# Optimization experiments

Hardware: AMD Instinct MI355X
Metric: run time of the kernel (lower is better)

## Reference

```python
import jax, jax.numpy as jnp
import numpy as np

B, S, D, H = 2, 2048, 1024, 16
DEPTH = D // H


def setup_inputs() -> dict:
    key = jax.random.key(0)
    ks = jax.random.split(key, 8)
    w_scale = 0.02
    # causal mask: 1.0 where attention is NOT allowed (added as mask * -1e9)
    causal = jnp.triu(jnp.ones((S, S), dtype=jnp.float32), k=1)[None, None]  # [1,1,S,S]
    return {
        "q": jax.random.normal(ks[0], (B, S, D), dtype=jnp.float32),
        "k": jax.random.normal(ks[1], (B, S, D), dtype=jnp.float32),
        "v": jax.random.normal(ks[2], (B, S, D), dtype=jnp.float32),
        "mask": causal,
        "Wq": jax.random.normal(ks[3], (D, D), dtype=jnp.float32) * w_scale,
        "bq": jnp.zeros((D,), dtype=jnp.float32),
        "Wk": jax.random.normal(ks[4], (D, D), dtype=jnp.float32) * w_scale,
        "bk": jnp.zeros((D,), dtype=jnp.float32),
        "Wv": jax.random.normal(ks[5], (D, D), dtype=jnp.float32) * w_scale,
        "bv": jnp.zeros((D,), dtype=jnp.float32),
        "Wo": jax.random.normal(ks[6], (D, D), dtype=jnp.float32) * w_scale,
        "bo": jnp.zeros((D,), dtype=jnp.float32),
    }


def _split_heads(x):
    # [B,S,D] -> [B,H,S,depth]
    return x.reshape(B, S, H, DEPTH).transpose(0, 2, 1, 3)


def reference(q, k, v, mask, Wq, bq, Wk, bk, Wv, bv, Wo, bo):
    qh = _split_heads(q @ Wq + bq)
    kh = _split_heads(k @ Wk + bk)
    vh = _split_heads(v @ Wv + bv)
    scale = 1.0 / jnp.sqrt(jnp.asarray(DEPTH, dtype=qh.dtype))
    logits = jnp.einsum('bhqd,bhkd->bhqk', qh, kh) * scale  # [B,H,S,S]
    logits = logits + mask * (-1e9)
    attn = jax.nn.softmax(logits, axis=-1)
    out = jnp.einsum('bhqk,bhkd->bhqd', attn, vh)  # [B,H,S,depth]
    out = out.transpose(0, 2, 1, 3).reshape(B, S, D)
    return out @ Wo + bo
```

## Files before the change

kernel.cpp:

```cpp
#include <hip/hip_runtime.h>


typedef unsigned short u16;
typedef unsigned int u32;

using bf16x8 = __attribute__((ext_vector_type(8))) short;
using f32x4  = __attribute__((ext_vector_type(4))) float;

#define SEQ 2048
#define DMODEL 1024
#define NHEAD 16
#define DEPTH 64
#define BATCH 2
#define M_ROWS (BATCH * SEQ)

__device__ __forceinline__ u16 f2bf(float f) {
    union { float f; u32 u; } v; v.f = f;
    u32 u = v.u;
    return (u16)((u + 0x7FFFu + ((u >> 16) & 1u)) >> 16);
}
__device__ __forceinline__ u16 f2bf_trunc(float f) {
    union { float f; u32 u; } v; v.f = f;
    return (u16)(v.u >> 16);
}

__device__ __forceinline__ f32x4 mfma16(bf16x8 a, bf16x8 b, f32x4 c) {
    return __builtin_amdgcn_mfma_f32_16x16x32_bf16(a, b, c, 0, 0, 0);
}

__device__ __forceinline__ void glds16(const u16* src, u16* dst) {
    __builtin_amdgcn_global_load_lds((const __attribute__((address_space(1))) void*)src,
                                     (__attribute__((address_space(3))) void*)dst,
                                     16, 0, 0);
}

__device__ __forceinline__ bf16x8 fragld(const u16* base, int lr, int gc) {
    return *(const bf16x8*)(base + lr * 64 + (((gc ^ lr) & 7) << 3));
}

__global__ void cvt3_kernel(const float* __restrict__ q, const float* __restrict__ k,
                            const float* __restrict__ v,
                            u16* __restrict__ qo, u16* __restrict__ ko, u16* __restrict__ vo) {
    const float* in; u16* out;
    if (blockIdx.z == 0)      { in = q; out = qo; }
    else if (blockIdx.z == 1) { in = k; out = ko; }
    else                      { in = v; out = vo; }
    int idx = blockIdx.x * blockDim.x + threadIdx.x;
    float4 val = ((const float4*)in)[idx];
    ushort4 o;
    o.x = f2bf(val.x); o.y = f2bf(val.y); o.z = f2bf(val.z); o.w = f2bf(val.w);
    ((ushort4*)out)[idx] = o;
}

__global__ void wtrans_kernel(const float* __restrict__ Wq, const float* __restrict__ Wk,
                              const float* __restrict__ Wv, const float* __restrict__ Wo,
                              u16* __restrict__ Wqt, u16* __restrict__ Wkt,
                              u16* __restrict__ Wvt, u16* __restrict__ Wot) {
    __shared__ float tile[32][33];
    const float* W; u16* Wt;
    switch (blockIdx.z) {
        case 0: W = Wq; Wt = Wqt; break;
        case 1: W = Wk; Wt = Wkt; break;
        case 2: W = Wv; Wt = Wvt; break;
        default: W = Wo; Wt = Wot; break;
    }
    int k0 = blockIdx.x * 32, n0 = blockIdx.y * 32;
    int tx = threadIdx.x, ty = threadIdx.y;
#pragma unroll
    for (int i = 0; i < 4; ++i)
        tile[ty + 8 * i][tx] = W[(size_t)(k0 + ty + 8 * i) * DMODEL + n0 + tx];
    __syncthreads();
#pragma unroll
    for (int i = 0; i < 4; ++i)
        Wt[(size_t)(n0 + ty + 8 * i) * DMODEL + k0 + tx] = f2bf(tile[tx][ty + 8 * i]);
}

template<int TM>
__device__ __forceinline__ void gemm_core(const u16* __restrict__ A, const u16* __restrict__ Bt,
                                          const float* __restrict__ bias,
                                          u16* __restrict__ outb, float* __restrict__ outf,
                                          int mode, float oscale, int bm0, int bn0) {
    constexpr int K = DMODEL;
    constexpr int MI = TM / 32;
    __shared__ u16 As[TM * 64];
    __shared__ u16 Bs[128 * 64];
    int t = threadIdx.x;
    int w = t >> 6, lane = t & 63, l15 = lane & 15, quad = lane >> 4;
    int wm = (w >> 1) * (TM / 2), wn = (w & 1) * 64;
    int r8 = lane >> 3, g8 = lane & 7;
    int gswz = ((g8 ^ r8) << 3);
    f32x4 acc[MI][4] = {};

    for (int it = 0; it < K / 64; ++it) {
        int k0 = it * 64;
        __syncthreads();
#pragma unroll
        for (int c = 0; c < MI; ++c) {
            int ch = w * MI + c;
            glds16(A + (size_t)(bm0 + ch * 8 + r8) * K + k0 + gswz, As + ch * 512);
        }
#pragma unroll
        for (int c = 0; c < 4; ++c) {
            int ch = w * 4 + c;
            glds16(Bt + (size_t)(bn0 + ch * 8 + r8) * K + k0 + gswz, Bs + ch * 512);
        }
        __syncthreads();
#pragma unroll
        for (int kk = 0; kk < 2; ++kk) {
            bf16x8 af[MI], bfr[4];
#pragma unroll
            for (int i = 0; i < MI; ++i) af[i]  = fragld(As, wm + i * 16 + l15, kk * 4 + quad);
#pragma unroll
            for (int j = 0; j < 4;  ++j) bfr[j] = fragld(Bs, wn + j * 16 + l15, kk * 4 + quad);
#pragma unroll
            for (int i = 0; i < MI; ++i)
#pragma unroll
                for (int j = 0; j < 4; ++j)
                    acc[i][j] = mfma16(af[i], bfr[j], acc[i][j]);
        }
    }
#pragma unroll
    for (int i = 0; i < MI; ++i) {
        int row_g0 = bm0 + wm + i * 16 + quad * 4;
#pragma unroll
        for (int j = 0; j < 4; ++j) {
            int col_g = bn0 + wn + j * 16 + l15;
            float bsv = bias[col_g];
#pragma unroll
            for (int r = 0; r < 4; ++r) {
                float v = (acc[i][j][r] + bsv) * oscale;
                int rg = row_g0 + r;
                if (mode == 2) {
                    outf[(size_t)rg * DMODEL + col_g] = v;
                } else {
                    int b = rg >> 11, s = rg & (SEQ - 1);
                    int h = col_g >> 6, d = col_g & 63;
                    size_t idx;
                    if (mode == 0) idx = ((size_t)(b * NHEAD + h) * SEQ + s) * DEPTH + d;
                    else           idx = ((size_t)(b * NHEAD + h) * DEPTH + d) * SEQ + s;
                    outb[idx] = f2bf(v);
                }
            }
        }
    }
}

#define SCALE_Q 0.1803368801111204f

__global__ __launch_bounds__(256) void gemm_qkv(
        const u16* __restrict__ qb, const u16* __restrict__ kb, const u16* __restrict__ vb,
        const u16* __restrict__ Wqt, const u16* __restrict__ Wkt, const u16* __restrict__ Wvt,
        const float* __restrict__ bq, const float* __restrict__ bk, const float* __restrict__ bv,
        u16* __restrict__ Qp, u16* __restrict__ Kp, u16* __restrict__ Vpt) {
    int id = blockIdx.x;
    int c = id & 7, m = id >> 3;
    int slab = c * 12 + (m >> 3);
    int x = m & 7;
    int z = slab >> 5, y = slab & 31;
    int bm0 = y * 128, bn0 = x * 128;
    if (z == 0)      gemm_core<128>(qb, Wqt, bq, Qp,  nullptr, 0, SCALE_Q, bm0, bn0);
    else if (z == 1) gemm_core<128>(kb, Wkt, bk, Kp,  nullptr, 0, 1.0f,    bm0, bn0);
    else             gemm_core<128>(vb, Wvt, bv, Vpt, nullptr, 1, 1.0f,    bm0, bn0);
}

__global__ __launch_bounds__(256) void gemm_out(
        const u16* __restrict__ attnb, const u16* __restrict__ Wot,
        const float* __restrict__ bo, float* __restrict__ out) {
    int id = blockIdx.x;
    int c = id & 7, m = id >> 3;
    int slab = c * 8 + (m >> 3);
    int x = m & 7;
    gemm_core<64>(attnb, Wot, bo, nullptr, out, 2, 1.0f, slab * 64, x * 128);
}

#define LP 72
__global__ __launch_bounds__(256) void attn_kernel(
        const u16* __restrict__ Qp, const u16* __restrict__ Kp,
        const u16* __restrict__ Vpt, u16* __restrict__ attn_out, u32* __restrict__ ctrs) {
    __shared__ u16 Klds[2][64 * 64];
    __shared__ u16 Vtlds[2][64 * 64];
    __shared__ u16 Plds[4 * 16 * LP];
    __shared__ u32 item_s;
    int t = threadIdx.x, w = t >> 6, lane = t & 63, l15 = lane & 15, quad = lane >> 4;
    int r8 = lane >> 3, g8 = lane & 7;
    int gswz = ((g8 ^ r8) << 3);
    u16* Pw = Plds + w * 16 * LP;
    int xcd = blockIdx.x & 7;
    u32* my_ctr = ctrs + xcd * 32;

    bf16x8 ones;
#pragma unroll
    for (int i = 0; i < 8; ++i) ones[i] = (short)0x3F80;

    for (;;) {
        if (t == 0) item_s = atomicAdd(my_ctr, 1);
        __syncthreads();
        u32 item = item_s;
        if (item >= 128) break;
        int qt = 31 - (int)(item >> 2);
        int bh = xcd * 4 + (int)(item & 3);
        int q0 = qt * 64;
        int nkt = qt + 1;
        int b = bh >> 4, h = bh & 15;
        const u16* Qbase = Qp  + (size_t)bh * SEQ * DEPTH;
        const u16* Kbase = Kp  + (size_t)bh * SEQ * DEPTH;
        const u16* Vbase = Vpt + (size_t)bh * DEPTH * SEQ;

        int qrow = q0 + w * 16 + l15;
        bf16x8 qf[2];
        qf[0] = *(const bf16x8*)(Qbase + (size_t)qrow * DEPTH + quad * 8);
        qf[1] = *(const bf16x8*)(Qbase + (size_t)qrow * DEPTH + 32 + quad * 8);

        f32x4 of[4] = {};
        f32x4 lacc = {};

#pragma unroll
        for (int c2 = 0; c2 < 2; ++c2) {
            int ch = w * 2 + c2;
            glds16(Kbase + (size_t)(ch * 8 + r8) * DEPTH + gswz, Klds[0] + ch * 512);
            glds16(Vbase + (size_t)(ch * 8 + r8) * SEQ + gswz,   Vtlds[0] + ch * 512);
        }

        for (int kt = 0; kt < nkt; ++kt) {
            int cur = kt & 1;
            __syncthreads();
            if (kt + 1 < nkt) {
                int nx = cur ^ 1, kn = kt + 1;
#pragma unroll
                for (int c2 = 0; c2 < 2; ++c2) {
                    int ch = w * 2 + c2;
                    glds16(Kbase + (size_t)(kn * 64 + ch * 8 + r8) * DEPTH + gswz,
                           Klds[nx] + ch * 512);
                    glds16(Vbase + (size_t)(ch * 8 + r8) * SEQ + kn * 64 + gswz,
                           Vtlds[nx] + ch * 512);
                }
            }
            f32x4 sc[4] = {};
#pragma unroll
            for (int nt = 0; nt < 4; ++nt)
#pragma unroll
                for (int kk = 0; kk < 2; ++kk)
                    sc[nt] = mfma16(qf[kk], fragld(Klds[cur], nt * 16 + l15, kk * 4 + quad), sc[nt]);

            bool diag = (kt == nkt - 1);
#pragma unroll
            for (int nt = 0; nt < 4; ++nt) {
#pragma unroll
                for (int r = 0; r < 4; ++r) {
                    float e = exp2f(sc[nt][r]);
                    if (diag) {
                        int col = nt * 16 + l15, row_ = w * 16 + quad * 4 + r;
                        e = (col > row_) ? 0.f : e;
                    }
                    Pw[(quad * 4 + r) * LP + nt * 16 + l15] = f2bf_trunc(e);
                }
            }
            bf16x8 pf[2];
            pf[0] = *(const bf16x8*)(Pw + l15 * LP + quad * 8);
            pf[1] = *(const bf16x8*)(Pw + l15 * LP + 32 + quad * 8);
#pragma unroll
            for (int kk = 0; kk < 2; ++kk) {
                lacc = mfma16(pf[kk], ones, lacc);
#pragma unroll
                for (int nt = 0; nt < 4; ++nt)
                    of[nt] = mfma16(pf[kk], fragld(Vtlds[cur], nt * 16 + l15, kk * 4 + quad), of[nt]);
            }
        }
#pragma unroll
        for (int r = 0; r < 4; ++r) {
            float inv = 1.0f / lacc[r];
            int s_ = q0 + w * 16 + quad * 4 + r;
#pragma unroll
            for (int nt = 0; nt < 4; ++nt) {
                int dcol = h * DEPTH + nt * 16 + l15;
                attn_out[((size_t)(b * SEQ + s_)) * DMODEL + dcol] = f2bf(of[nt][r] * inv);
            }
        }
    }
}

extern "C" void kernel_launch(void* const* d_in, const int* in_sizes, int n_in,
                              void* d_out, int out_size, void* d_ws, size_t ws_size,
                              hipStream_t stream) {
    const float* q  = (const float*)d_in[0];
    const float* k  = (const float*)d_in[1];
    const float* v  = (const float*)d_in[2];
    const float* Wq = (const float*)d_in[4];
    const float* bq = (const float*)d_in[5];
    const float* Wk = (const float*)d_in[6];
    const float* bk = (const float*)d_in[7];
    const float* Wv = (const float*)d_in[8];
    const float* bv = (const float*)d_in[9];
    const float* Wo = (const float*)d_in[10];
    const float* bo = (const float*)d_in[11];
    float* out = (float*)d_out;

    char* ws = (char*)d_ws;
    const size_t SZ_ACT = (size_t)M_ROWS * DMODEL * 2;
    const size_t SZ_W   = (size_t)DMODEL * DMODEL * 2;
    u16* qb   = (u16*)(ws);
    u16* kb   = (u16*)(ws + SZ_ACT);
    u16* vb   = (u16*)(ws + 2 * SZ_ACT);
    u16* Wqt  = (u16*)(ws + 3 * SZ_ACT);
    u16* Wkt  = (u16*)(ws + 3 * SZ_ACT + SZ_W);
    u16* Wvt  = (u16*)(ws + 3 * SZ_ACT + 2 * SZ_W);
    u16* Wot  = (u16*)(ws + 3 * SZ_ACT + 3 * SZ_W);
    u16* Qp   = (u16*)(ws + 3 * SZ_ACT + 4 * SZ_W);
    u16* Kp   = (u16*)(ws + 4 * SZ_ACT + 4 * SZ_W);
    u16* Vpt  = (u16*)(ws + 5 * SZ_ACT + 4 * SZ_W);
    u16* attnb= (u16*)(ws + 6 * SZ_ACT + 4 * SZ_W);
    u32* ctrs = (u32*)(ws + 7 * SZ_ACT + 4 * SZ_W);

    hipMemsetAsync(ctrs, 0, 1024, stream);
    cvt3_kernel<<<dim3(4096, 1, 3), 256, 0, stream>>>(q, k, v, qb, kb, vb);
    wtrans_kernel<<<dim3(32, 32, 4), dim3(32, 8), 0, stream>>>(Wq, Wk, Wv, Wo, Wqt, Wkt, Wvt, Wot);
    gemm_qkv<<<dim3(768), 256, 0, stream>>>(
        qb, kb, vb, Wqt, Wkt, Wvt, bq, bk, bv, Qp, Kp, Vpt);
    attn_kernel<<<dim3(768), 256, 0, stream>>>(Qp, Kp, Vpt, attnb, ctrs);
    gemm_out<<<dim3(512), 256, 0, stream>>>(attnb, Wot, bo, out);
}
```

Before: 237.3 us.

## Rewrite QKV projection GEMM as 256x256 tiles with 8-phase ping-pong pipeline

The QKV projection GEMM moves from 128x128 tiles with 256 threads to 256x256 tiles with 512 threads. It uses a double-buffered LDS layout split into halves, and an eight-phase schedule that interleaves global-to-LDS staging with MFMA phases under barriers and raised priority. The aim is more data reuse per tile and better overlap of memory with compute. The cost is only 192 blocks, which may underfill the GPU's CUs. It also uses a large LDS footprint and high register pressure from 32 accumulators per thread.

```diff
diff --git a/kernel.cpp b/kernel.cpp
--- a/kernel.cpp
+++ b/kernel.cpp
@@ -36,6 +36,12 @@
 
 __device__ __forceinline__ bf16x8 fragld(const u16* base, int lr, int gc) {
     return *(const bf16x8*)(base + lr * 64 + (((gc ^ lr) & 7) << 3));
+}
+
+__device__ __forceinline__ void xbar() {
+    asm volatile("" ::: "memory");
+    __builtin_amdgcn_s_barrier();
+    asm volatile("" ::: "memory");
 }
 
 __global__ void cvt3_kernel(const float* __restrict__ q, const float* __restrict__ k,
@@ -147,20 +153,101 @@
 
 #define SCALE_Q 0.1803368801111204f
 
-__global__ __launch_bounds__(256) void gemm_qkv(
+
+#define STAGE_A(P, h, kt) do { \
+    glds16(A  + (size_t)(bm0 + (h)*128 + (w*2  )*8 + r8) * DMODEL + (kt)*64 + gswz, &Ah[P][h][(w*2  )*512]); \
+    glds16(A  + (size_t)(bm0 + (h)*128 + (w*2+1)*8 + r8) * DMODEL + (kt)*64 + gswz, &Ah[P][h][(w*2+1)*512]); } while(0)
+#define STAGE_B(P, h, kt) do { \
+    glds16(Bt + (size_t)(bn0 + (h)*128 + (w*2  )*8 + r8) * DMODEL + (kt)*64 + gswz, &Bh[P][h][(w*2  )*512]); \
+    glds16(Bt + (size_t)(bn0 + (h)*128 + (w*2+1)*8 + r8) * DMODEL + (kt)*64 + gswz, &Bh[P][h][(w*2+1)*512]); } while(0)
+#define LOAD_BF(P) do { \
+    _Pragma("unroll") for (int nj = 0; nj < 4; ++nj) \
+    _Pragma("unroll") for (int kk = 0; kk < 2; ++kk) \
+        bf[nj][kk] = fragld(&Bh[P][bhf][0], brow0 + nj * 16 + l15, kk * 4 + quad); } while(0)
+#define LOAD_AF(P, q) do { \
+    _Pragma("unroll") for (int i = 0; i < 2; ++i) \
+    _Pragma("unroll") for (int kk = 0; kk < 2; ++kk) \
+        af[i][kk] = fragld(&Ah[P][wm][0], ((q)*2 + i) * 16 + l15, kk * 4 + quad); } while(0)
+#define MFMA_PH(q) do { \
+    __builtin_amdgcn_s_setprio(1); \
+    _Pragma("unroll") for (int kk = 0; kk < 2; ++kk) \
+    _Pragma("unroll") for (int i = 0; i < 2; ++i) \
+    _Pragma("unroll") for (int nj = 0; nj < 4; ++nj) \
+        acc[(q)*2 + i][nj] = mfma16(af[i][kk], bf[nj][kk], acc[(q)*2 + i][nj]); \
+    __builtin_amdgcn_s_setprio(0); } while(0)
+#define VMW4() asm volatile("s_waitcnt vmcnt(4)" ::: "memory")
+
+__global__ __launch_bounds__(512, 2) void gemm_qkv(
         const u16* __restrict__ qb, const u16* __restrict__ kb, const u16* __restrict__ vb,
         const u16* __restrict__ Wqt, const u16* __restrict__ Wkt, const u16* __restrict__ Wvt,
         const float* __restrict__ bq, const float* __restrict__ bk, const float* __restrict__ bv,
         u16* __restrict__ Qp, u16* __restrict__ Kp, u16* __restrict__ Vpt) {
+    __shared__ u16 Ah[2][2][128 * 64];
+    __shared__ u16 Bh[2][2][128 * 64];
+
     int id = blockIdx.x;
     int c = id & 7, m = id >> 3;
-    int slab = c * 12 + (m >> 3);
-    int x = m & 7;
-    int z = slab >> 5, y = slab & 31;
-    int bm0 = y * 128, bn0 = x * 128;
-    if (z == 0)      gemm_core<128>(qb, Wqt, bq, Qp,  nullptr, 0, SCALE_Q, bm0, bn0);
-    else if (z == 1) gemm_core<128>(kb, Wkt, bk, Kp,  nullptr, 0, 1.0f,    bm0, bn0);
-    else             gemm_core<128>(vb, Wvt, bv, Vpt, nullptr, 1, 1.0f,    bm0, bn0);
+    int t0 = c * 24 + m;
+    int z = t0 >> 6, rem = t0 & 63;
+    int y = rem >> 2, x = rem & 3;
+    int bm0 = y * 256, bn0 = x * 256;
+
+    const u16* A; const u16* Bt; const float* bias; u16* outb; int mode; float oscale;
+    if (z == 0)      { A = qb; Bt = Wqt; bias = bq; outb = Qp;  mode = 0; oscale = SCALE_Q; }
+    else if (z == 1) { A = kb; Bt = Wkt; bias = bk; outb = Kp;  mode = 0; oscale = 1.0f; }
+    else             { A = vb; Bt = Wvt; bias = bv; outb = Vpt; mode = 1; oscale = 1.0f; }
+
+    int tid = threadIdx.x;
+    int w = tid >> 6, lane = tid & 63, l15 = lane & 15, quad = lane >> 4;
+    int wm = w >> 2, wn = w & 3;
+    int bhf = wn >> 1, brow0 = (wn & 1) << 6;
+    int r8 = lane >> 3, g8 = lane & 7;
+    int gswz = ((g8 ^ r8) << 3);
+
+    f32x4 acc[8][4] = {};
+    bf16x8 bf[4][2], af[2][2];
+
+    STAGE_B(0, 0, 0); STAGE_B(0, 1, 0);
+    STAGE_A(0, 0, 0); STAGE_A(0, 1, 0);
+    STAGE_B(1, 0, 1); STAGE_B(1, 1, 1);
+    VMW4();
+    xbar();
+
+    for (int j = 0; j < 8; ++j) {
+        int k2 = 2 * j;
+        int kc2 = (k2 + 2 < 16) ? k2 + 2 : 15;
+        int kc3 = (k2 + 3 < 16) ? k2 + 3 : 15;
+        LOAD_BF(0); LOAD_AF(0, 0); STAGE_A(1, 0, k2 + 1);          xbar(); MFMA_PH(0); xbar();
+        LOAD_AF(0, 1);             STAGE_A(1, 1, k2 + 1);          xbar(); MFMA_PH(1); xbar();
+        LOAD_AF(0, 2);             STAGE_B(0, 0, kc2);             xbar(); MFMA_PH(2); xbar();
+        LOAD_AF(0, 3);             STAGE_B(0, 1, kc2);    VMW4();  xbar(); MFMA_PH(3); xbar();
+        LOAD_BF(1); LOAD_AF(1, 0); STAGE_A(0, 0, kc2);             xbar(); MFMA_PH(0); xbar();
+        LOAD_AF(1, 1);             STAGE_A(0, 1, kc2);             xbar(); MFMA_PH(1); xbar();
+        LOAD_AF(1, 2);             STAGE_B(1, 0, kc3);             xbar(); MFMA_PH(2); xbar();
+        LOAD_AF(1, 3);             STAGE_B(1, 1, kc3);    VMW4();  xbar(); MFMA_PH(3); xbar();
+    }
+    asm volatile("s_waitcnt vmcnt(0)" ::: "memory");
+
+#pragma unroll
+    for (int mi = 0; mi < 8; ++mi) {
+        int row_g0 = bm0 + wm * 128 + mi * 16 + quad * 4;
+#pragma unroll
+        for (int nj = 0; nj < 4; ++nj) {
+            int col_g = bn0 + wn * 64 + nj * 16 + l15;
+            float bsv = bias[col_g];
+#pragma unroll
+            for (int r = 0; r < 4; ++r) {
+                float v = (acc[mi][nj][r] + bsv) * oscale;
+                int rg = row_g0 + r;
+                int b = rg >> 11, s = rg & (SEQ - 1);
+                int h = col_g >> 6, d = col_g & 63;
+                size_t idx;
+                if (mode == 0) idx = ((size_t)(b * NHEAD + h) * SEQ + s) * DEPTH + d;
+                else           idx = ((size_t)(b * NHEAD + h) * DEPTH + d) * SEQ + s;
+                outb[idx] = f2bf(v);
+            }
+        }
+    }
 }
 
 __global__ __launch_bounds__(256) void gemm_out(
@@ -314,7 +401,7 @@
     hipMemsetAsync(ctrs, 0, 1024, stream);
     cvt3_kernel<<<dim3(4096, 1, 3), 256, 0, stream>>>(q, k, v, qb, kb, vb);
     wtrans_kernel<<<dim3(32, 32, 4), dim3(32, 8), 0, stream>>>(Wq, Wk, Wv, Wo, Wqt, Wkt, Wvt, Wot);
-    gemm_qkv<<<dim3(768), 256, 0, stream>>>(
+    gemm_qkv<<<dim3(192), 512, 0, stream>>>(
         qb, kb, vb, Wqt, Wkt, Wvt, bq, bk, bv, Qp, Kp, Vpt);
     attn_kernel<<<dim3(768), 256, 0, stream>>>(Qp, Kp, Vpt, attnb, ctrs);
     gemm_out<<<dim3(512), 256, 0, stream>>>(attnb, Wot, bo, out);
```

After: 258.0 us. +8.7%, slower.

## Double-buffer LDS tiles in projection GEMM to overlap loads with MFMA

Applied to the files above, without the earlier changes.

Splits the A and B shared-memory tiles of the projection GEMM core into two buffers. The next K-tile is prefetched with global-to-LDS loads while MFMAs run on the current one, and one barrier per iteration replaces two. This targets the exposed global-load latency in the K loop. It doubles LDS use, which can lower occupancy, and correctness depends on the single barrier ordering the async LDS writes.

```diff
diff --git a/kernel.cpp b/kernel.cpp
--- a/kernel.cpp
+++ b/kernel.cpp
@@ -81,9 +81,10 @@
                                           u16* __restrict__ outb, float* __restrict__ outf,
                                           int mode, float oscale, int bm0, int bn0) {
     constexpr int K = DMODEL;
+    constexpr int NT = K / 64;
     constexpr int MI = TM / 32;
-    __shared__ u16 As[TM * 64];
-    __shared__ u16 Bs[128 * 64];
+    __shared__ u16 As[2][TM * 64];
+    __shared__ u16 Bs[2][128 * 64];
     int t = threadIdx.x;
     int w = t >> 6, lane = t & 63, l15 = lane & 15, quad = lane >> 4;
     int wm = (w >> 1) * (TM / 2), wn = (w & 1) * 64;
@@ -91,34 +92,38 @@
     int gswz = ((g8 ^ r8) << 3);
     f32x4 acc[MI][4] = {};
 
-    for (int it = 0; it < K / 64; ++it) {
-        int k0 = it * 64;
-        __syncthreads();
-#pragma unroll
-        for (int c = 0; c < MI; ++c) {
-            int ch = w * MI + c;
-            glds16(A + (size_t)(bm0 + ch * 8 + r8) * K + k0 + gswz, As + ch * 512);
-        }
-#pragma unroll
-        for (int c = 0; c < 4; ++c) {
-            int ch = w * 4 + c;
-            glds16(Bt + (size_t)(bn0 + ch * 8 + r8) * K + k0 + gswz, Bs + ch * 512);
-        }
-        __syncthreads();
+#define QSTAGE(p, kt) do { \
+    _Pragma("unroll") for (int c = 0; c < MI; ++c) { \
+        int ch = w * MI + c; \
+        glds16(A + (size_t)(bm0 + ch * 8 + r8) * K + (kt) * 64 + gswz, &As[p][ch * 512]); } \
+    _Pragma("unroll") for (int c = 0; c < 4; ++c) { \
+        int ch = w * 4 + c; \
+        glds16(Bt + (size_t)(bn0 + ch * 8 + r8) * K + (kt) * 64 + gswz, &Bs[p][ch * 512]); } \
+    } while (0)
+
+    QSTAGE(0, 0);
+    __syncthreads();
+
+    for (int kt = 0; kt < NT; ++kt) {
+        int cur = kt & 1;
+        if (kt + 1 < NT) QSTAGE(cur ^ 1, kt + 1);
 #pragma unroll
         for (int kk = 0; kk < 2; ++kk) {
             bf16x8 af[MI], bfr[4];
 #pragma unroll
-            for (int i = 0; i < MI; ++i) af[i]  = fragld(As, wm + i * 16 + l15, kk * 4 + quad);
-#pragma unroll
-            for (int j = 0; j < 4;  ++j) bfr[j] = fragld(Bs, wn + j * 16 + l15, kk * 4 + quad);
+            for (int i = 0; i < MI; ++i) af[i]  = fragld(&As[cur][0], wm + i * 16 + l15, kk * 4 + quad);
+#pragma unroll
+            for (int j = 0; j < 4;  ++j) bfr[j] = fragld(&Bs[cur][0], wn + j * 16 + l15, kk * 4 + quad);
 #pragma unroll
             for (int i = 0; i < MI; ++i)
 #pragma unroll
                 for (int j = 0; j < 4; ++j)
                     acc[i][j] = mfma16(af[i], bfr[j], acc[i][j]);
         }
+        __syncthreads();
     }
+#undef QSTAGE
+
 #pragma unroll
     for (int i = 0; i < MI; ++i) {
         int row_g0 = bm0 + wm + i * 16 + quad * 4;
```

Result: slower. 246.7 us (+4.0%).
